# Optimization experiments

Hardware: AMD Instinct MI355X
Metric: run time of the kernel (lower is better)

## Reference

```python
import jax, jax.numpy as jnp
import numpy as np

S, B, E, H = 1024, 4, 1024, 16
D = E // H  # head_dim = 64


def setup_inputs() -> dict:
    key = jax.random.key(0)
    ks = jax.random.split(key, 22)
    inp = {}
    names_io = ["query_r", "query_i", "key_r", "key_i", "value_r", "value_i"]
    for i, n in enumerate(names_io):
        inp[n] = jax.random.normal(ks[i], (S, B, E), dtype=jnp.float32)
    scale = 0.02
    j = 6
    for p in ["q", "k", "v", "o"]:
        inp[f"w{p}_r"] = jax.random.normal(ks[j], (E, E), dtype=jnp.float32) * scale; j += 1
        inp[f"w{p}_i"] = jax.random.normal(ks[j], (E, E), dtype=jnp.float32) * scale; j += 1
        inp[f"b{p}_r"] = jax.random.normal(ks[j], (E,), dtype=jnp.float32) * scale; j += 1
        inp[f"b{p}_i"] = jax.random.normal(ks[j], (E,), dtype=jnp.float32) * scale; j += 1
    return inp


def _clinear(x, wr, wi, br, bi):
    # complex linear: x @ W^T + b, torch Linear convention (weight [out,in])
    w = wr + 1j * wi
    b = br + 1j * bi
    return x @ w.T + b


def reference(query_r, query_i, key_r, key_i, value_r, value_i,
              wq_r, wq_i, bq_r, bq_i, wk_r, wk_i, bk_r, bk_i,
              wv_r, wv_i, bv_r, bv_i, wo_r, wo_i, bo_r, bo_i):
    # batch_first=False: inputs are [S, B, E] -> [B, S, E]
    q = jnp.transpose(query_r + 1j * query_i, (1, 0, 2))
    k = jnp.transpose(key_r + 1j * key_i, (1, 0, 2))
    v = jnp.transpose(value_r + 1j * value_i, (1, 0, 2))

    def heads(x):  # [B,S,E] -> [B,H,S,D]
        return jnp.transpose(x.reshape(B, S, H, D), (0, 2, 1, 3))

    Q = heads(_clinear(q, wq_r, wq_i, bq_r, bq_i))
    K = heads(_clinear(k, wk_r, wk_i, bk_r, bk_i))
    V = heads(_clinear(v, wv_r, wv_i, bv_r, bv_i))

    scores = jnp.einsum("bhqd,bhkd->bhqk", Q, K) / jnp.sqrt(jnp.float32(D))
    # split softmax: softmax over real and imag parts independently
    attn = (jax.nn.softmax(scores.real, axis=-1)
            + 1j * jax.nn.softmax(scores.imag, axis=-1))
    out = jnp.einsum("bhqk,bhkd->bhqd", attn, V)  # [B,H,S,D]
    out = jnp.transpose(out, (0, 2, 1, 3)).reshape(B, S, E)
    out = _clinear(out, wo_r, wo_i, bo_r, bo_i)
    out = jnp.transpose(out, (1, 0, 2))  # back to [S,B,E]
    # return complex output as stacked (real, imag) floats: [S,B,E,2]
    return jnp.stack([out.real, out.imag], axis=-1)
```

## Files before the change

### kernel.cpp

```cpp
#include <hip/hip_runtime.h>
#include <hip/hip_bf16.h>
#include <stdint.h>

#define S_LEN 1024
#define B_SZ  4
#define E_SZ  1024
#define H_CNT 16
#define D_HD  64
#define N1    (B_SZ * H_CNT * S_LEN * D_HD)
#define WELEM (E_SZ * E_SZ)

typedef __attribute__((ext_vector_type(8))) short short8;
typedef __attribute__((ext_vector_type(4))) float f32x4;

__device__ __forceinline__ ushort f2bf(float f) {
  union { float f; uint32_t u; } v; v.f = f;
  uint32_t u = v.u;
  uint32_t r = (u + 0x7fffu + ((u >> 16) & 1u)) >> 16;
  return (ushort)r;
}
__device__ __forceinline__ short8 pack8(float4 a, float4 b) {
  short8 r;
  r[0] = (short)f2bf(a.x); r[1] = (short)f2bf(a.y);
  r[2] = (short)f2bf(a.z); r[3] = (short)f2bf(a.w);
  r[4] = (short)f2bf(b.x); r[5] = (short)f2bf(b.y);
  r[6] = (short)f2bf(b.z); r[7] = (short)f2bf(b.w);
  return r;
}
static __device__ __forceinline__ f32x4 mfma16(short8 a, short8 b, f32x4 c) {
  return __builtin_amdgcn_mfma_f32_16x16x32_bf16(a, b, c, 0, 0, 0);
}

typedef const __attribute__((address_space(1))) void gv_t;
typedef __attribute__((address_space(3))) void lv_t;
__device__ __forceinline__ void gld16(const void* g, void* l) {
  __builtin_amdgcn_global_load_lds((gv_t*)g, (lv_t*)l, 16, 0, 0);
}

__global__ __launch_bounds__(256) void cast_all(
    const float* __restrict__ s0, const float* __restrict__ s1,
    const float* __restrict__ s2, const float* __restrict__ s3,
    const float* __restrict__ s4, const float* __restrict__ s5,
    const float* __restrict__ s6, const float* __restrict__ s7,
    ushort* __restrict__ wdst,
    const float* __restrict__ qr, const float* __restrict__ qi,
    const float* __restrict__ kr, const float* __restrict__ ki,
    const float* __restrict__ vr, const float* __restrict__ vi,
    ushort* __restrict__ xq_r, ushort* __restrict__ xq_i,
    ushort* __restrict__ xk_r, ushort* __restrict__ xk_i,
    ushort* __restrict__ xv_r, ushort* __restrict__ xv_i)
{
  int blk = blockIdx.x;
  if (blk < 8192) {
    const size_t i = (size_t)blk * 256 + threadIdx.x;
    const size_t e = i * 4;
    const int which = (int)(e >> 20);
    const size_t off = e & (WELEM - 1);
    const float* s = which < 4
        ? (which < 2 ? (which == 0 ? s0 : s1) : (which == 2 ? s2 : s3))
        : (which < 6 ? (which == 4 ? s4 : s5) : (which == 6 ? s6 : s7));
    const float4 f = *(const float4*)(s + off);
    ushort4 u;
    u.x = f2bf(f.x); u.y = f2bf(f.y); u.z = f2bf(f.z); u.w = f2bf(f.w);
    *(ushort4*)(wdst + e) = u;
    return;
  }
  blk -= 8192;
  const float *xr, *xi; ushort *yr, *yi;
  if      (blk < 2048) { xr = qr; xi = qi; yr = xq_r; yi = xq_i; }
  else if (blk < 4096) { xr = kr; xi = ki; yr = xk_r; yi = xk_i; blk -= 2048; }
  else                 { xr = vr; xi = vi; yr = xv_r; yi = xv_i; blk -= 4096; }
  const size_t e = ((size_t)blk * 256 + threadIdx.x) * 8;
  float4 a = *(const float4*)(xr + e);
  float4 b = *(const float4*)(xr + e + 4);
  *(short8*)(yr + e) = pack8(a, b);
  a = *(const float4*)(xi + e);
  b = *(const float4*)(xi + e + 4);
  *(short8*)(yi + e) = pack8(a, b);
}

__global__ __launch_bounds__(256) void cgemm_qkv3(
    const ushort* __restrict__ a0r, const ushort* __restrict__ a0i,
    const ushort* __restrict__ a1r, const ushort* __restrict__ a1i,
    const ushort* __restrict__ a2r, const ushort* __restrict__ a2i,
    const ushort* __restrict__ w0r, const ushort* __restrict__ w0i,
    const ushort* __restrict__ w1r, const ushort* __restrict__ w1i,
    const ushort* __restrict__ w2r, const ushort* __restrict__ w2i,
    const float* __restrict__ b0r, const float* __restrict__ b0i,
    const float* __restrict__ b1r, const float* __restrict__ b1i,
    const float* __restrict__ b2r, const float* __restrict__ b2i,
    ushort* __restrict__ y0r, ushort* __restrict__ y0i,
    ushort* __restrict__ y1r, ushort* __restrict__ y1i,
    ushort* __restrict__ y2r, ushort* __restrict__ y2i,
    float qscale)
{
  __shared__ __align__(16) ushort sAr[128 * 64], sAi[128 * 64];
  __shared__ __align__(16) ushort sBr[64 * 64],  sBi[64 * 64];

  const int z = blockIdx.z;
  const ushort* ar_ = (z == 0) ? a0r : (z == 1) ? a1r : a2r;
  const ushort* ai_ = (z == 0) ? a0i : (z == 1) ? a1i : a2i;
  const ushort* wre = (z == 0) ? w0r : (z == 1) ? w1r : w2r;
  const ushort* wim = (z == 0) ? w0i : (z == 1) ? w1i : w2i;
  const float*  bre = (z == 0) ? b0r : (z == 1) ? b1r : b2r;
  const float*  bim = (z == 0) ? b0i : (z == 1) ? b1i : b2i;
  ushort* yr = (z == 0) ? y0r : (z == 1) ? y1r : y2r;
  ushort* yi = (z == 0) ? y0i : (z == 1) ? y1i : y2i;
  const float scale = (z == 0) ? qscale : 1.0f;

  const int tid  = threadIdx.x;
  const int lane = tid & 63;
  const int w    = tid >> 6;
  const int wrow = w >> 1, wcol = w & 1;
  const int fr   = lane & 15, fq = lane >> 4;

  const int flat = blockIdx.x + gridDim.x * blockIdx.y;
  const int swz  = (flat & 7) * 64 + (flat >> 3);
  const int n0   = (swz & 15) * 64;
  const int m0   = (swz >> 4) * 128;

  const ushort* gbase = (w == 0) ? ar_ : (w == 1) ? ai_ : (w == 2) ? wre : wim;
  char* sbase = (w == 0) ? (char*)sAr : (w == 1) ? (char*)sAi
              : (w == 2) ? (char*)sBr : (char*)sBi;
  const int rbase = (w < 2) ? m0 : n0;
  const int lrow  = lane >> 3;
  const int sch   = (lane & 7) ^ lrow;
  const ushort* gp0 = gbase + (size_t)(rbase + lrow) * E_SZ + sch * 8;

  f32x4 accR[4][2] = {}, accI[4][2] = {};

  for (int kt = 0; kt < 16; ++kt) {
    const int k0 = kt * 64;
    __syncthreads();
    if (w < 2) {
#pragma unroll
      for (int i = 0; i < 16; ++i)
        gld16(gp0 + (size_t)i * 8 * E_SZ + k0, sbase + i * 1024);
    } else {
#pragma unroll
      for (int i = 0; i < 8; ++i)
        gld16(gp0 + (size_t)i * 8 * E_SZ + k0, sbase + i * 1024);
    }
    __syncthreads();

#pragma unroll
    for (int kk = 0; kk < 2; ++kk) {
      short8 a_r[4], a_i[4], a_n[4], b_r[2], b_i[2];
#pragma unroll
      for (int mi = 0; mi < 4; ++mi) {
        const int row = wrow * 64 + mi * 16 + fr;
        const int off = row * 128 + (((kk * 4 + fq) ^ (row & 7)) << 4);
        a_r[mi] = *(const short8*)((const char*)sAr + off);
        a_i[mi] = *(const short8*)((const char*)sAi + off);
        a_n[mi] = a_i[mi] ^ (short)0x8000;
      }
#pragma unroll
      for (int ni = 0; ni < 2; ++ni) {
        const int row = wcol * 32 + ni * 16 + fr;
        const int off = row * 128 + (((kk * 4 + fq) ^ (row & 7)) << 4);
        b_r[ni] = *(const short8*)((const char*)sBr + off);
        b_i[ni] = *(const short8*)((const char*)sBi + off);
      }
      __builtin_amdgcn_s_setprio(1);
#pragma unroll
      for (int mi = 0; mi < 4; ++mi)
#pragma unroll
        for (int ni = 0; ni < 2; ++ni) {
          accR[mi][ni] = mfma16(a_r[mi], b_r[ni], accR[mi][ni]);
          accR[mi][ni] = mfma16(a_n[mi], b_i[ni], accR[mi][ni]);
          accI[mi][ni] = mfma16(a_r[mi], b_i[ni], accI[mi][ni]);
          accI[mi][ni] = mfma16(a_i[mi], b_r[ni], accI[mi][ni]);
        }
      __builtin_amdgcn_s_setprio(0);
    }
  }

#pragma unroll
  for (int ni = 0; ni < 2; ++ni) {
    const int n = n0 + wcol * 32 + ni * 16 + fr;
    const float bR = bre[n], bI = bim[n];
    const int h = n >> 6, d = n & 63;
#pragma unroll
    for (int mi = 0; mi < 4; ++mi) {
      const int mb = m0 + wrow * 64 + mi * 16 + fq * 4;
#pragma unroll
      for (int q = 0; q < 4; ++q) {
        const int m = mb + q;
        const float vr = (accR[mi][ni][q] + bR) * scale;
        const float vi = (accI[mi][ni][q] + bI) * scale;
        const int s = m >> 2, b = m & 3;
        size_t o;
        if (z < 2) o = (((size_t)(b * H_CNT + h) * S_LEN) + s) * D_HD + d;
        else       o = (((size_t)(b * H_CNT + h) * D_HD) + d) * S_LEN + s;
        yr[o] = f2bf(vr); yi[o] = f2bf(vi);
      }
    }
  }
}

__global__ __launch_bounds__(256) void cgemm_o(
    const ushort* __restrict__ ar_, const ushort* __restrict__ ai_,
    const ushort* __restrict__ wre, const ushort* __restrict__ wim,
    const float* __restrict__ bre, const float* __restrict__ bim,
    float* __restrict__ outf)
{
  __shared__ __align__(16) ushort sAr[128 * 64], sAi[128 * 64];
  __shared__ __align__(16) ushort sBr[64 * 64],  sBi[64 * 64];

  const int tid  = threadIdx.x;
  const int lane = tid & 63;
  const int w    = tid >> 6;
  const int wrow = w >> 1, wcol = w & 1;
  const int fr   = lane & 15, fq = lane >> 4;

  const int flat = blockIdx.x + gridDim.x * blockIdx.y;
  const int swz  = (flat & 7) * 64 + (flat >> 3);
  const int n0   = (swz & 15) * 64;
  const int m0   = (swz >> 4) * 128;

  const ushort* gbase = (w == 0) ? ar_ : (w == 1) ? ai_ : (w == 2) ? wre : wim;
  char* sbase = (w == 0) ? (char*)sAr : (w == 1) ? (char*)sAi
              : (w == 2) ? (char*)sBr : (char*)sBi;
  const int rbase = (w < 2) ? m0 : n0;
  const int lrow  = lane >> 3;
  const int sch   = (lane & 7) ^ lrow;
  const ushort* gp0 = gbase + (size_t)(rbase + lrow) * E_SZ + sch * 8;

  f32x4 accR[4][2] = {}, accI[4][2] = {};

  for (int kt = 0; kt < 16; ++kt) {
    const int k0 = kt * 64;
    __syncthreads();
    if (w < 2) {
#pragma unroll
      for (int i = 0; i < 16; ++i)
        gld16(gp0 + (size_t)i * 8 * E_SZ + k0, sbase + i * 1024);
    } else {
#pragma unroll
      for (int i = 0; i < 8; ++i)
        gld16(gp0 + (size_t)i * 8 * E_SZ + k0, sbase + i * 1024);
    }
    __syncthreads();

#pragma unroll
    for (int kk = 0; kk < 2; ++kk) {
      short8 a_r[4], a_i[4], a_n[4], b_r[2], b_i[2];
#pragma unroll
      for (int mi = 0; mi < 4; ++mi) {
        const int row = wrow * 64 + mi * 16 + fr;
        const int off = row * 128 + (((kk * 4 + fq) ^ (row & 7)) << 4);
        a_r[mi] = *(const short8*)((const char*)sAr + off);
        a_i[mi] = *(const short8*)((const char*)sAi + off);
        a_n[mi] = a_i[mi] ^ (short)0x8000;
      }
#pragma unroll
      for (int ni = 0; ni < 2; ++ni) {
        const int row = wcol * 32 + ni * 16 + fr;
        const int off = row * 128 + (((kk * 4 + fq) ^ (row & 7)) << 4);
        b_r[ni] = *(const short8*)((const char*)sBr + off);
        b_i[ni] = *(const short8*)((const char*)sBi + off);
      }
      __builtin_amdgcn_s_setprio(1);
#pragma unroll
      for (int mi = 0; mi < 4; ++mi)
#pragma unroll
        for (int ni = 0; ni < 2; ++ni) {
          accR[mi][ni] = mfma16(a_r[mi], b_r[ni], accR[mi][ni]);
          accR[mi][ni] = mfma16(a_n[mi], b_i[ni], accR[mi][ni]);
          accI[mi][ni] = mfma16(a_r[mi], b_i[ni], accI[mi][ni]);
          accI[mi][ni] = mfma16(a_i[mi], b_r[ni], accI[mi][ni]);
        }
      __builtin_amdgcn_s_setprio(0);
    }
  }

#pragma unroll
  for (int ni = 0; ni < 2; ++ni) {
    const int n = n0 + wcol * 32 + ni * 16 + fr;
    const float bR = bre[n], bI = bim[n];
#pragma unroll
    for (int mi = 0; mi < 4; ++mi) {
      const int mb = m0 + wrow * 64 + mi * 16 + fq * 4;
#pragma unroll
      for (int q = 0; q < 4; ++q) {
        const int m = mb + q;
        const int b = m >> 10, s = m & 1023;
        const size_t o = (((size_t)(s * B_SZ + b) * E_SZ) + n) * 2;
        outf[o]     = accR[mi][ni][q] + bR;
        outf[o + 1] = accI[mi][ni][q] + bI;
      }
    }
  }
}

__global__ __launch_bounds__(256, 3) void cattn_mfma(
    const ushort* __restrict__ Qr, const ushort* __restrict__ Qi,
    const ushort* __restrict__ Kr, const ushort* __restrict__ Ki,
    const ushort* __restrict__ Vtr, const ushort* __restrict__ Vti,
    ushort* __restrict__ AOr, ushort* __restrict__ AOi)
{
  __shared__ __align__(16) ushort sK[2][64][64];
  __shared__ __align__(16) ushort sVt[2][64][64];
  __shared__ __align__(16) ushort sP[4][2][16][64];

  const int tid  = threadIdx.x;
  const int lane = tid & 63;
  const int w    = tid >> 6;
  const int g    = lane >> 4;
  const int fr   = lane & 15;

  const int id   = blockIdx.x;
  const int xcd  = id & 7;
  const int loc  = id >> 3;
  const int bh   = (xcd << 3) | (loc & 7);
  const int q0   = (loc >> 3) << 6;
  const int b    = bh >> 4, h = bh & 15;
  const int qw   = q0 + 16 * w;

  short8 qfr[2], qfi[2];
  const size_t qrow = ((size_t)bh * S_LEN + qw + fr) * D_HD;
#pragma unroll
  for (int kk = 0; kk < 2; ++kk) {
    qfr[kk] = *(const short8*)(Qr + qrow + kk * 32 + g * 8);
    qfi[kk] = *(const short8*)(Qi + qrow + kk * 32 + g * 8);
  }

  const int lrow8 = lane >> 3;
  const int sch   = (lane & 7) ^ lrow8;
  const ushort* gsrc; ushort* sdst;
  if      (w == 0) { gsrc = Kr  + (size_t)bh * S_LEN * D_HD; sdst = &sK[0][0][0]; }
  else if (w == 1) { gsrc = Ki  + (size_t)bh * S_LEN * D_HD; sdst = &sK[1][0][0]; }
  else if (w == 2) { gsrc = Vtr + (size_t)bh * D_HD * S_LEN; sdst = &sVt[0][0][0]; }
  else             { gsrc = Vti + (size_t)bh * D_HD * S_LEN; sdst = &sVt[1][0][0]; }
  const bool isK = (w < 2);

  f32x4 accA[4] = {}, accAi[4] = {}, accB[4] = {}, accBi[4] = {};
  float lpr = 0.f, lpi = 0.f;

  ushort* pR = &sP[w][0][0][0];
  ushort* pI = &sP[w][1][0][0];

  for (int kt = 0; kt < 16; ++kt) {
    __syncthreads();
    if (isK) {
      const ushort* gp = gsrc + (size_t)kt * 4096 + lrow8 * 64 + sch * 8;
#pragma unroll
      for (int i = 0; i < 8; ++i)
        gld16(gp + i * 512, (char*)sdst + i * 1024);
    } else {
      const ushort* gp = gsrc + (size_t)lrow8 * S_LEN + kt * 64 + sch * 8;
#pragma unroll
      for (int i = 0; i < 8; ++i)
        gld16(gp + (size_t)i * 8 * S_LEN, (char*)sdst + i * 1024);
    }
    __syncthreads();

    f32x4 Sr[4] = {}, Si[4] = {};
#pragma unroll
    for (int n = 0; n < 4; ++n) {
      const int kc = fr + 16 * n;
      const int rb = kc * 128, sw = (kc & 7) << 4;
#pragma unroll
      for (int kk = 0; kk < 2; ++kk) {
        const int off = rb + ((((kk * 4 + g) << 4)) ^ sw);
        short8 krf = *(const short8*)((const char*)&sK[0][0][0] + off);
        short8 kif = *(const short8*)((const char*)&sK[1][0][0] + off);
        short8 kin = kif ^ (short)0x8000;
        Sr[n] = mfma16(krf, qfr[kk], Sr[n]);
        Sr[n] = mfma16(kin, qfi[kk], Sr[n]);
        Si[n] = mfma16(kif, qfr[kk], Si[n]);
        Si[n] = mfma16(krf, qfi[kk], Si[n]);
      }
    }

    const int pbase = fr * 128 + ((g & 1) << 3);
#pragma unroll
    for (int n = 0; n < 4; ++n) {
      float p0 = __builtin_amdgcn_exp2f(Sr[n][0]);
      float p1 = __builtin_amdgcn_exp2f(Sr[n][1]);
      float p2 = __builtin_amdgcn_exp2f(Sr[n][2]);
      float p3 = __builtin_amdgcn_exp2f(Sr[n][3]);
      float q0_ = __builtin_amdgcn_exp2f(Si[n][0]);
      float q1_ = __builtin_amdgcn_exp2f(Si[n][1]);
      float q2_ = __builtin_amdgcn_exp2f(Si[n][2]);
      float q3_ = __builtin_amdgcn_exp2f(Si[n][3]);
      lpr += (p0 + p1) + (p2 + p3);
      lpi += (q0_ + q1_) + (q2_ + q3_);
      uint32_t a0, a1, b0, b1;
      asm("v_cvt_pk_bf16_f32 %0, %1, %2" : "=v"(a0) : "v"(p0), "v"(p1));
      asm("v_cvt_pk_bf16_f32 %0, %1, %2" : "=v"(a1) : "v"(p2), "v"(p3));
      asm("v_cvt_pk_bf16_f32 %0, %1, %2" : "=v"(b0) : "v"(q0_), "v"(q1_));
      asm("v_cvt_pk_bf16_f32 %0, %1, %2" : "=v"(b1) : "v"(q2_), "v"(q3_));
      const int chunk = (2 * n + (g >> 1)) ^ (fr & 7);
      const int off = pbase + (chunk << 4);
      uint2 pa; pa.x = a0; pa.y = a1;
      uint2 pb; pb.x = b0; pb.y = b1;
      *(uint2*)((char*)pR + off) = pa;
      *(uint2*)((char*)pI + off) = pb;
    }
    asm volatile("s_waitcnt lgkmcnt(0)" ::: "memory");

    short8 prf[2], pif[2];
#pragma unroll
    for (int kk = 0; kk < 2; ++kk) {
      const int off = fr * 128 + ((((kk * 4 + g) << 4)) ^ ((fr & 7) << 4));
      prf[kk] = *(const short8*)((const char*)pR + off);
      pif[kk] = *(const short8*)((const char*)pI + off);
    }
#pragma unroll
    for (int n = 0; n < 4; ++n) {
      const int d = fr + 16 * n;
      const int rb = d * 128, sw = (d & 7) << 4;
#pragma unroll
      for (int kk = 0; kk < 2; ++kk) {
        const int off = rb + ((((kk * 4 + g) << 4)) ^ sw);
        short8 vrf = *(const short8*)((const char*)&sVt[0][0][0] + off);
        short8 vif = *(const short8*)((const char*)&sVt[1][0][0] + off);
        accA [n] = mfma16(prf[kk], vrf, accA [n]);
        accAi[n] = mfma16(prf[kk], vif, accAi[n]);
        accB [n] = mfma16(pif[kk], vrf, accB [n]);
        accBi[n] = mfma16(pif[kk], vif, accBi[n]);
      }
    }
  }

  lpr += __shfl_xor(lpr, 16); lpr += __shfl_xor(lpr, 32);
  lpi += __shfl_xor(lpi, 16); lpi += __shfl_xor(lpi, 32);
  f32x4 ilr, ili;
#pragma unroll
  for (int t = 0; t < 4; ++t) {
    const int src = (lane & 48) + (g << 2) + t;
    ilr[t] = 1.f / __shfl(lpr, src, 64);
    ili[t] = 1.f / __shfl(lpi, src, 64);
  }

#pragma unroll
  for (int n = 0; n < 4; ++n) {
    const int e = h * 64 + fr + 16 * n;
#pragma unroll
    for (int t = 0; t < 4; ++t) {
      const int sidx = qw + g * 4 + t;
      const size_t o = ((size_t)b * S_LEN + sidx) * E_SZ + e;
      AOr[o] = f2bf(accA [n][t] * ilr[t] - accBi[n][t] * ili[t]);
      AOi[o] = f2bf(accAi[n][t] * ilr[t] + accB [n][t] * ili[t]);
    }
  }
}

extern "C" void kernel_launch(void* const* d_in, const int* in_sizes, int n_in,
                              void* d_out, int out_size, void* d_ws, size_t ws_size,
                              hipStream_t stream)
{
    const float* query_r = (const float*)d_in[0];
    const float* query_i = (const float*)d_in[1];
    const float* key_r   = (const float*)d_in[2];
    const float* key_i   = (const float*)d_in[3];
    const float* value_r = (const float*)d_in[4];
    const float* value_i = (const float*)d_in[5];
    const float* wq_r = (const float*)d_in[6];
    const float* wq_i = (const float*)d_in[7];
    const float* bq_r = (const float*)d_in[8];
    const float* bq_i = (const float*)d_in[9];
    const float* wk_r = (const float*)d_in[10];
    const float* wk_i = (const float*)d_in[11];
    const float* bk_r = (const float*)d_in[12];
    const float* bk_i = (const float*)d_in[13];
    const float* wv_r = (const float*)d_in[14];
    const float* wv_i = (const float*)d_in[15];
    const float* bv_r = (const float*)d_in[16];
    const float* bv_i = (const float*)d_in[17];
    const float* wo_r = (const float*)d_in[18];
    const float* wo_i = (const float*)d_in[19];
    const float* bo_r = (const float*)d_in[20];
    const float* bo_i = (const float*)d_in[21];

    ushort* ws   = (ushort*)d_ws;
    ushort* Qr   = ws;
    ushort* Qi   = Qr + (size_t)N1;
    ushort* Kr   = Qi + (size_t)N1;
    ushort* Ki   = Kr + (size_t)N1;
    ushort* Vtr  = Ki + (size_t)N1;
    ushort* Vti  = Vtr + (size_t)N1;
    ushort* Wb   = Vti + (size_t)N1;
    ushort* Wq_r = Wb + 0 * (size_t)WELEM;
    ushort* Wq_i = Wb + 1 * (size_t)WELEM;
    ushort* Wk_r = Wb + 2 * (size_t)WELEM;
    ushort* Wk_i = Wb + 3 * (size_t)WELEM;
    ushort* Wv_r = Wb + 4 * (size_t)WELEM;
    ushort* Wv_i = Wb + 5 * (size_t)WELEM;
    ushort* Wo_r = Wb + 6 * (size_t)WELEM;
    ushort* Wo_i = Wb + 7 * (size_t)WELEM;
    ushort* AOr  = Wb + 8 * (size_t)WELEM;
    ushort* AOi  = AOr + (size_t)N1;

    ushort* Xq_r = (ushort*)d_out;
    ushort* Xq_i = Xq_r + (size_t)N1;
    ushort* Xk_r = Xq_i + (size_t)N1;
    ushort* Xk_i = Xk_r + (size_t)N1;
    ushort* Xv_r = AOr;
    ushort* Xv_i = AOi;

    cast_all<<<14336, 256, 0, stream>>>(
        wq_r, wq_i, wk_r, wk_i, wv_r, wv_i, wo_r, wo_i, Wb,
        query_r, query_i, key_r, key_i, value_r, value_i,
        Xq_r, Xq_i, Xk_r, Xk_i, Xv_r, Xv_i);

    dim3 gg3(16, 32, 3);
    cgemm_qkv3<<<gg3, 256, 0, stream>>>(
        Xq_r, Xq_i, Xk_r, Xk_i, Xv_r, Xv_i,
        Wq_r, Wq_i, Wk_r, Wk_i, Wv_r, Wv_i,
        bq_r, bq_i, bk_r, bk_i, bv_r, bv_i,
        Qr, Qi, Kr, Ki, Vtr, Vti,
        0.18033688011112043f);

    cattn_mfma<<<1024, 256, 0, stream>>>(
        Qr, Qi, Kr, Ki, Vtr, Vti, AOr, AOi);

    cgemm_o<<<dim3(16, 32), 256, 0, stream>>>(
        AOr, AOi, Wo_r, Wo_i, bo_r, bo_i, (float*)d_out);
}
```

Baseline: 262.5 us.

## Split QKV GEMM into Q/K and V launches and register-prefetch attention tiles

The fused three-way QKV projection is split into a Q/K kernel with interleaved block scheduling and a separate templated V GEMM that writes transposed output. The output projection reuses the same template. In the attention kernel, the direct global-to-LDS loads are replaced by register staging that prefetches the next K/V tile while the current one is computed, so load latency can overlap with compute. This adds register pressure in a kernel launched with occupancy 3 and adds an extra kernel launch.

```diff
diff --git a/kernel.cpp b/kernel.cpp
--- a/kernel.cpp
+++ b/kernel.cpp
@@ -79,34 +79,16 @@
   *(short8*)(yi + e) = pack8(a, b);
 }
 
-__global__ __launch_bounds__(256) void cgemm_qkv3(
-    const ushort* __restrict__ a0r, const ushort* __restrict__ a0i,
-    const ushort* __restrict__ a1r, const ushort* __restrict__ a1i,
-    const ushort* __restrict__ a2r, const ushort* __restrict__ a2i,
-    const ushort* __restrict__ w0r, const ushort* __restrict__ w0i,
-    const ushort* __restrict__ w1r, const ushort* __restrict__ w1i,
-    const ushort* __restrict__ w2r, const ushort* __restrict__ w2i,
-    const float* __restrict__ b0r, const float* __restrict__ b0i,
-    const float* __restrict__ b1r, const float* __restrict__ b1i,
-    const float* __restrict__ b2r, const float* __restrict__ b2i,
-    ushort* __restrict__ y0r, ushort* __restrict__ y0i,
-    ushort* __restrict__ y1r, ushort* __restrict__ y1i,
-    ushort* __restrict__ y2r, ushort* __restrict__ y2i,
-    float qscale)
+template<int MODE>
+__global__ __launch_bounds__(256) void cgemm(
+    const ushort* __restrict__ ar_, const ushort* __restrict__ ai_,
+    const ushort* __restrict__ wre, const ushort* __restrict__ wim,
+    const float* __restrict__ bre, const float* __restrict__ bim,
+    ushort* __restrict__ yr, ushort* __restrict__ yi,
+    float* __restrict__ outf, float scale)
 {
   __shared__ __align__(16) ushort sAr[128 * 64], sAi[128 * 64];
   __shared__ __align__(16) ushort sBr[64 * 64],  sBi[64 * 64];
-
-  const int z = blockIdx.z;
-  const ushort* ar_ = (z == 0) ? a0r : (z == 1) ? a1r : a2r;
-  const ushort* ai_ = (z == 0) ? a0i : (z == 1) ? a1i : a2i;
-  const ushort* wre = (z == 0) ? w0r : (z == 1) ? w1r : w2r;
-  const ushort* wim = (z == 0) ? w0i : (z == 1) ? w1i : w2i;
-  const float*  bre = (z == 0) ? b0r : (z == 1) ? b1r : b2r;
-  const float*  bim = (z == 0) ? b0i : (z == 1) ? b1i : b2i;
-  ushort* yr = (z == 0) ? y0r : (z == 1) ? y1r : y2r;
-  ushort* yi = (z == 0) ? y0i : (z == 1) ? y1i : y2i;
-  const float scale = (z == 0) ? qscale : 1.0f;
 
   const int tid  = threadIdx.x;
   const int lane = tid & 63;
@@ -188,24 +170,51 @@
         const int m = mb + q;
         const float vr = (accR[mi][ni][q] + bR) * scale;
         const float vi = (accI[mi][ni][q] + bI) * scale;
-        const int s = m >> 2, b = m & 3;
-        size_t o;
-        if (z < 2) o = (((size_t)(b * H_CNT + h) * S_LEN) + s) * D_HD + d;
-        else       o = (((size_t)(b * H_CNT + h) * D_HD) + d) * S_LEN + s;
-        yr[o] = f2bf(vr); yi[o] = f2bf(vi);
-      }
-    }
-  }
-}
-
-__global__ __launch_bounds__(256) void cgemm_o(
-    const ushort* __restrict__ ar_, const ushort* __restrict__ ai_,
-    const ushort* __restrict__ wre, const ushort* __restrict__ wim,
-    const float* __restrict__ bre, const float* __restrict__ bim,
-    float* __restrict__ outf)
+        if (MODE == 0) {
+          const int s = m >> 2, b = m & 3;
+          const size_t o = (((size_t)(b * H_CNT + h) * S_LEN) + s) * D_HD + d;
+          yr[o] = f2bf(vr); yi[o] = f2bf(vi);
+        } else if (MODE == 1) {
+          const int s = m >> 2, b = m & 3;
+          const size_t o = (((size_t)(b * H_CNT + h) * D_HD) + d) * S_LEN + s;
+          yr[o] = f2bf(vr); yi[o] = f2bf(vi);
+        } else {
+          const int b = m >> 10, s = m & 1023;
+          const size_t o = (((size_t)(s * B_SZ + b) * E_SZ) + n) * 2;
+          outf[o] = vr; outf[o + 1] = vi;
+        }
+      }
+    }
+  }
+}
+
+__global__ __launch_bounds__(256) void cgemm_qk(
+    const ushort* __restrict__ aQr, const ushort* __restrict__ aQi,
+    const ushort* __restrict__ aKr, const ushort* __restrict__ aKi,
+    const ushort* __restrict__ wQr, const ushort* __restrict__ wQi,
+    const ushort* __restrict__ wKr, const ushort* __restrict__ wKi,
+    const float* __restrict__ bQr, const float* __restrict__ bQi,
+    const float* __restrict__ bKr, const float* __restrict__ bKi,
+    ushort* __restrict__ yQr, ushort* __restrict__ yQi,
+    ushort* __restrict__ yKr, ushort* __restrict__ yKi,
+    float qscale)
 {
   __shared__ __align__(16) ushort sAr[128 * 64], sAi[128 * 64];
   __shared__ __align__(16) ushort sBr[64 * 64],  sBi[64 * 64];
+
+  const int id    = blockIdx.x;
+  const int isKop = (id >> 2) & 1;
+  const int lid   = ((id >> 3) << 2) | (id & 3);
+
+  const ushort* ar_ = isKop ? aKr : aQr;
+  const ushort* ai_ = isKop ? aKi : aQi;
+  const ushort* wre = isKop ? wKr : wQr;
+  const ushort* wim = isKop ? wKi : wQi;
+  const float*  bre = isKop ? bKr : bQr;
+  const float*  bim = isKop ? bKi : bQi;
+  ushort* yr = isKop ? yKr : yQr;
+  ushort* yi = isKop ? yKi : yQi;
+  const float scale = isKop ? 1.0f : qscale;
 
   const int tid  = threadIdx.x;
   const int lane = tid & 63;
@@ -213,8 +222,7 @@
   const int wrow = w >> 1, wcol = w & 1;
   const int fr   = lane & 15, fq = lane >> 4;
 
-  const int flat = blockIdx.x + gridDim.x * blockIdx.y;
-  const int swz  = (flat & 7) * 64 + (flat >> 3);
+  const int swz  = (lid & 3) * 128 + (lid >> 2);
   const int n0   = (swz & 15) * 64;
   const int m0   = (swz >> 4) * 128;
 
@@ -278,16 +286,18 @@
   for (int ni = 0; ni < 2; ++ni) {
     const int n = n0 + wcol * 32 + ni * 16 + fr;
     const float bR = bre[n], bI = bim[n];
+    const int h = n >> 6, d = n & 63;
 #pragma unroll
     for (int mi = 0; mi < 4; ++mi) {
       const int mb = m0 + wrow * 64 + mi * 16 + fq * 4;
 #pragma unroll
       for (int q = 0; q < 4; ++q) {
         const int m = mb + q;
-        const int b = m >> 10, s = m & 1023;
-        const size_t o = (((size_t)(s * B_SZ + b) * E_SZ) + n) * 2;
-        outf[o]     = accR[mi][ni][q] + bR;
-        outf[o + 1] = accI[mi][ni][q] + bI;
+        const float vr = (accR[mi][ni][q] + bR) * scale;
+        const float vi = (accI[mi][ni][q] + bI) * scale;
+        const int s = m >> 2, b = m & 3;
+        const size_t o = (((size_t)(b * H_CNT + h) * S_LEN) + s) * D_HD + d;
+        yr[o] = f2bf(vr); yi[o] = f2bf(vi);
       }
     }
   }
@@ -340,20 +350,35 @@
   ushort* pR = &sP[w][0][0][0];
   ushort* pI = &sP[w][1][0][0];
 
+  uint4 stg[8];
+  if (isK) {
+    const ushort* gp = gsrc + lrow8 * 64 + sch * 8;
+#pragma unroll
+    for (int i = 0; i < 8; ++i) stg[i] = *(const uint4*)(gp + i * 512);
+  } else {
+    const ushort* gp = gsrc + (size_t)lrow8 * S_LEN + sch * 8;
+#pragma unroll
+    for (int i = 0; i < 8; ++i) stg[i] = *(const uint4*)(gp + (size_t)i * 8 * S_LEN);
+  }
+
   for (int kt = 0; kt < 16; ++kt) {
     __syncthreads();
-    if (isK) {
-      const ushort* gp = gsrc + (size_t)kt * 4096 + lrow8 * 64 + sch * 8;
-#pragma unroll
-      for (int i = 0; i < 8; ++i)
-        gld16(gp + i * 512, (char*)sdst + i * 1024);
-    } else {
-      const ushort* gp = gsrc + (size_t)lrow8 * S_LEN + kt * 64 + sch * 8;
-#pragma unroll
-      for (int i = 0; i < 8; ++i)
-        gld16(gp + (size_t)i * 8 * S_LEN, (char*)sdst + i * 1024);
-    }
+#pragma unroll
+    for (int i = 0; i < 8; ++i)
+      *(uint4*)((char*)sdst + (size_t)lane * 16 + i * 1024) = stg[i];
     __syncthreads();
+
+    if (kt < 15) {
+      if (isK) {
+        const ushort* gp = gsrc + (size_t)(kt + 1) * 4096 + lrow8 * 64 + sch * 8;
+#pragma unroll
+        for (int i = 0; i < 8; ++i) stg[i] = *(const uint4*)(gp + i * 512);
+      } else {
+        const ushort* gp = gsrc + (size_t)lrow8 * S_LEN + (kt + 1) * 64 + sch * 8;
+#pragma unroll
+        for (int i = 0; i < 8; ++i) stg[i] = *(const uint4*)(gp + (size_t)i * 8 * S_LEN);
+      }
+    }
 
     f32x4 Sr[4] = {}, Si[4] = {};
 #pragma unroll
@@ -505,17 +530,20 @@
         query_r, query_i, key_r, key_i, value_r, value_i,
         Xq_r, Xq_i, Xk_r, Xk_i, Xv_r, Xv_i);
 
-    dim3 gg3(16, 32, 3);
-    cgemm_qkv3<<<gg3, 256, 0, stream>>>(
-        Xq_r, Xq_i, Xk_r, Xk_i, Xv_r, Xv_i,
-        Wq_r, Wq_i, Wk_r, Wk_i, Wv_r, Wv_i,
-        bq_r, bq_i, bk_r, bk_i, bv_r, bv_i,
-        Qr, Qi, Kr, Ki, Vtr, Vti,
+    cgemm_qk<<<1024, 256, 0, stream>>>(
+        Xq_r, Xq_i, Xk_r, Xk_i,
+        Wq_r, Wq_i, Wk_r, Wk_i,
+        bq_r, bq_i, bk_r, bk_i,
+        Qr, Qi, Kr, Ki,
         0.18033688011112043f);
+
+    dim3 gg(16, 32);
+    cgemm<1><<<gg, 256, 0, stream>>>(Xv_r, Xv_i, Wv_r, Wv_i, bv_r, bv_i,
+                                     Vtr, Vti, nullptr, 1.0f);
 
     cattn_mfma<<<1024, 256, 0, stream>>>(
         Qr, Qi, Kr, Ki, Vtr, Vti, AOr, AOi);
 
-    cgemm_o<<<dim3(16, 32), 256, 0, stream>>>(
-        AOr, AOi, Wo_r, Wo_i, bo_r, bo_i, (float*)d_out);
-}
+    cgemm<2><<<gg, 256, 0, stream>>>(
+        AOr, AOi, Wo_r, Wo_i, bo_r, bo_i, nullptr, nullptr, (float*)d_out, 1.0f);
+}
```

Result: slower. 388.4 us (+48.0%).
